# Kernel optimization log

Measured on AMD Instinct MI355X. Metric: run time of the kernel, lower is better.

The kernel has to match this reference:

```python
import jax, jax.numpy as jnp
import numpy as np

EMBED_DIM = 1024
N_HEADS = 16
HEAD_DIM = EMBED_DIM // N_HEADS

def setup_inputs() -> dict:
    key = jax.random.key(0)
    kx, kq, kk, kv, ko = jax.random.split(key, 5)
    s = 1.0 / np.sqrt(EMBED_DIM)
    return {
        "x": jax.random.normal(kx, (4, 2048, EMBED_DIM), dtype=jnp.float32),
        "Wq": jax.random.normal(kq, (EMBED_DIM, EMBED_DIM), dtype=jnp.float32) * s,
        "Wk": jax.random.normal(kk, (EMBED_DIM, EMBED_DIM), dtype=jnp.float32) * s,
        "Wv": jax.random.normal(kv, (EMBED_DIM, EMBED_DIM), dtype=jnp.float32) * s,
        "Wo": jax.random.normal(ko, (EMBED_DIM, EMBED_DIM), dtype=jnp.float32) * s,
    }

def reference(x, Wq, Wk, Wv, Wo):
    B, T, D = x.shape
    H, Dh = N_HEADS, HEAD_DIM
    # projections (nn.Linear: y = x @ W.T); split heads -> [B, H, T, Dh]
    Q = (x @ Wq.T).reshape(B, T, H, Dh).transpose(0, 2, 1, 3)
    K = (x @ Wk.T).reshape(B, T, H, Dh).transpose(0, 2, 1, 3)
    V = (x @ Wv.T).reshape(B, T, H, Dh).transpose(0, 2, 1, 3)
    scores = jnp.einsum("bhqd,bhkd->bhqk", Q, K) / jnp.sqrt(jnp.float32(Dh))
    attn = jax.nn.softmax(scores, axis=-1)
    out = jnp.einsum("bhqk,bhkd->bhqd", attn, V)  # [B,H,T,Dh]
    out = out.transpose(0, 2, 1, 3).reshape(B, T, D)
    return out @ Wo.T
```

## Files before the change

kernel.cpp:

```cpp
#include <hip/hip_runtime.h>

typedef _Float16 f16;
typedef _Float16 f16x8 __attribute__((ext_vector_type(8)));
typedef _Float16 f16x4 __attribute__((ext_vector_type(4)));
typedef float f32x4 __attribute__((ext_vector_type(4)));

#define MFMA16(a, b, c) __builtin_amdgcn_mfma_f32_16x16x32_f16((a), (b), (c), 0, 0, 0)
#define MEMBAR() __asm__ __volatile__("" ::: "memory")

__device__ __forceinline__ void cp16(const f16* g, f16* l) {
  __builtin_amdgcn_global_load_lds(
      (const __attribute__((address_space(1))) void*)g,
      (__attribute__((address_space(3))) void*)l, 16, 0, 0);
}

__global__ __launch_bounds__(256) void cvt_all(
    const float* __restrict__ x,  const float* __restrict__ Wq,
    const float* __restrict__ Wk, const float* __restrict__ Wv,
    const float* __restrict__ Wo,
    f16* __restrict__ X16, f16* __restrict__ Wq16, f16* __restrict__ Wk16,
    f16* __restrict__ Wv16, f16* __restrict__ Wo16) {
  int blk = blockIdx.x;
  const float* src; f16* dst; size_t off;
  if (blk < 4096) { src = x; dst = X16; off = (size_t)blk * 2048; }
  else {
    int t = blk - 4096, widx = t >> 9, loc = t & 511;
    src = (widx == 0) ? Wq : (widx == 1) ? Wk : (widx == 2) ? Wv : Wo;
    dst = (widx == 0) ? Wq16 : (widx == 1) ? Wk16 : (widx == 2) ? Wv16 : Wo16;
    off = (size_t)loc * 2048;
  }
  size_t e = off + (size_t)threadIdx.x * 8;
  const float4* s = (const float4*)(src + e);
  float4 a = s[0], b = s[1];
  f16x8 o;
  o[0] = (f16)a.x; o[1] = (f16)a.y; o[2] = (f16)a.z; o[3] = (f16)a.w;
  o[4] = (f16)b.x; o[5] = (f16)b.y; o[6] = (f16)b.z; o[7] = (f16)b.w;
  *(f16x8*)(dst + e) = o;
}

__device__ __forceinline__ void gemm_core(
    const f16* __restrict__ A, const f16* __restrict__ B, void* __restrict__ Cv,
    bool outF16, bool permT, int N, int K, int bm, int bn, float scale,
    f16* As, f16* Bs) {
  const int tid = threadIdx.x;
  const int lane = tid & 63, w = tid >> 6;
  const int wm = w >> 1, wn = w & 1;
  const int c = lane & 15, q = lane >> 4;
  const int key = (c >> 1) & 3;
  f32x4 acc[4][4] = {};

  const int Lrow = lane >> 2, Lp = (lane & 3) ^ ((lane >> 3) & 3);
  auto stage = [&](int k0, int bufi) {
#pragma unroll
    for (int j = 0; j < 2; ++j) {
      int r0 = (w * 2 + j) * 16;
      cp16(A + (size_t)(bm + r0 + Lrow) * K + k0 + Lp * 8,
           As + bufi * 4096 + r0 * 32 + lane * 8);
    }
#pragma unroll
    for (int j = 0; j < 2; ++j) {
      int r0 = (w * 2 + j) * 16;
      cp16(B + (size_t)(bn + r0 + Lrow) * K + k0 + Lp * 8,
           Bs + bufi * 4096 + r0 * 32 + lane * 8);
    }
  };

  stage(0, 0);
  const int NIT = K >> 5;
  for (int i = 0; i < NIT; ++i) {
    if (i + 1 < NIT) {
      stage((i + 1) << 5, (i + 1) & 1);
      __builtin_amdgcn_s_waitcnt(0x0F74);
    } else {
      __builtin_amdgcn_s_waitcnt(0x0F70);
    }
    __builtin_amdgcn_s_barrier();
    MEMBAR();
    const f16* Ab = As + (i & 1) * 4096;
    const f16* Bb = Bs + (i & 1) * 4096;
    f16x8 af[4], bf[4];
#pragma unroll
    for (int mt = 0; mt < 4; ++mt)
      af[mt] = *(const f16x8*)(Ab + (wm * 64 + mt * 16 + c) * 32 + (q ^ key) * 8);
#pragma unroll
    for (int nt = 0; nt < 4; ++nt)
      bf[nt] = *(const f16x8*)(Bb + (wn * 64 + nt * 16 + c) * 32 + (q ^ key) * 8);
#pragma unroll
    for (int mt = 0; mt < 4; ++mt)
#pragma unroll
      for (int nt = 0; nt < 4; ++nt)
        acc[mt][nt] = MFMA16(af[mt], bf[nt], acc[mt][nt]);
    MEMBAR();
    __builtin_amdgcn_s_barrier();
  }

#pragma unroll
  for (int mt = 0; mt < 4; ++mt)
#pragma unroll
    for (int nt = 0; nt < 4; ++nt)
#pragma unroll
      for (int r = 0; r < 4; ++r) {
        size_t row = bm + wm * 64 + mt * 16 + q * 4 + r;
        size_t col = bn + wn * 64 + nt * 16 + c;
        if (permT) {
          int t = (int)col & 63;
          col = (col & ~(size_t)63) |
                (size_t)((t & 0x23) | ((t & 0x0C) << 1) | ((t & 0x10) >> 2));
        }
        float v = acc[mt][nt][r] * scale;
        if (outF16) ((f16*)Cv)[row * N + col] = (f16)v;
        else ((float*)Cv)[row * N + col] = v;
      }
}

__global__ __launch_bounds__(256, 4) void gemm_qkvt(
    const f16* __restrict__ X, const f16* __restrict__ Wq,
    const f16* __restrict__ Wk, const f16* __restrict__ Wv,
    f16* __restrict__ Q, f16* __restrict__ Ko, f16* __restrict__ VT, float cs) {
  __shared__ __align__(16) f16 As[8192], Bs[8192];
  const int z = blockIdx.z, x = blockIdx.x;
  if (z < 2) {
    gemm_core(X, z ? Wk : Wq, z ? (void*)Ko : (void*)Q, true, false, 1024, 1024,
              (x >> 3) * 128, (x & 7) * 128, z ? 1.0f : cs, As, Bs);
  } else {
    gemm_core(Wv, X, (void*)VT, true, true, 8192, 1024,
              (x >> 6) * 128, (x & 63) * 128, 1.0f, As, Bs);
  }
}

__global__ __launch_bounds__(256, 4) void gemm_o(
    const f16* __restrict__ A, const f16* __restrict__ Wo, float* __restrict__ out) {
  __shared__ __align__(16) f16 As[8192], Bs[8192];
  const int x = blockIdx.x;
  gemm_core(A, Wo, (void*)out, false, false, 1024, 1024,
            (x >> 3) * 128, (x & 7) * 128, 1.0f, As, Bs);
}

__global__ __launch_bounds__(512, 4) void attn_kernel(
    const f16* __restrict__ Qg, const f16* __restrict__ Kg,
    const f16* __restrict__ VTg, f16* __restrict__ Og) {
  const int T = 2048, D = 1024;
  const int x = blockIdx.x;
  const int xcd = x & 7, rem = x >> 3;
  const int qt = rem & 7, grp = rem >> 3;
  const int bh = (grp << 3) | xcd;
  const int b = bh >> 4, h = bh & 15;
  const size_t base = ((size_t)b * T) * D + h * 64;
  const size_t baseV = (size_t)h * 64 * 8192 + (size_t)b * T;
  __shared__ __align__(16) f16 smem[16384];
  const int tid = threadIdx.x;
  const int lane = tid & 63, w = tid >> 6;
  const int c = lane & 15, q = lane >> 4;
  const int cx = c & 7;
  f16* Kb = smem;
  f16* Vb = smem + 8192;

#pragma unroll
  for (int j = 0; j < 4; ++j) {
    int cb = (w * 4 + j) * 64;
    int ch = cb + lane;
    int row = ch >> 3, p = (ch & 7) ^ (row & 7);
    cp16(Qg + base + (size_t)(qt * 256 + row) * D + p * 8, smem + cb * 8);
  }
  __syncthreads();
  f16x8 qf[2][2];
#pragma unroll
  for (int nt = 0; nt < 2; ++nt)
#pragma unroll
    for (int kh = 0; kh < 2; ++kh)
      qf[nt][kh] = *(const f16x8*)(smem + (w * 32 + nt * 16 + c) * 64 + ((kh * 4 + q) ^ cx) * 8);
  __syncthreads();

  float l_[2] = {0.f, 0.f};
  f32x4 o_[2][4] = {};

  auto stageKV = [&](int kv, int bufi) {
    f16* Ks = Kb + bufi * 4096;
    f16* Vt = Vb + bufi * 4096;
    int cb = w * 64;
    int ch = cb + lane;
    int row = ch >> 3, p = (ch & 7) ^ (row & 7);
    cp16(Kg + base + (size_t)(kv + row) * D + p * 8, Ks + cb * 8);
    cp16(VTg + baseV + (size_t)row * 8192 + kv + p * 8, Vt + cb * 8);
  };

  stageKV(0, 0);
  for (int i = 0; i < 32; ++i) {
    if (i < 31) {
      stageKV((i + 1) * 64, (i + 1) & 1);
      __builtin_amdgcn_s_waitcnt(0x0F72);
    } else {
      __builtin_amdgcn_s_waitcnt(0x0F70);
    }
    __builtin_amdgcn_s_barrier();

    f16* Ks = Kb + (i & 1) * 4096;
    f16* Vt = Vb + (i & 1) * 4096;

    f32x4 st[4][2] = {};
#pragma unroll
    for (int kh = 0; kh < 2; ++kh) {
      f16x8 kf[4];
#pragma unroll
      for (int mt = 0; mt < 4; ++mt)
        kf[mt] = *(const f16x8*)(Ks + (mt * 16 + c) * 64 + ((kh * 4 + q) ^ cx) * 8);
      __builtin_amdgcn_s_setprio(1);
#pragma unroll
      for (int mt = 0; mt < 4; ++mt)
#pragma unroll
        for (int g = 0; g < 2; ++g)
          st[mt][g] = MFMA16(kf[mt], qf[g][kh], st[mt][g]);
      __builtin_amdgcn_s_setprio(0);
    }

    f16x8 pf[2][2];
#pragma unroll
    for (int g = 0; g < 2; ++g) {
      float s = 0.f;
#pragma unroll
      for (int mt = 0; mt < 4; ++mt) {
        float p0 = __builtin_amdgcn_exp2f(st[mt][g][0]);
        float p1 = __builtin_amdgcn_exp2f(st[mt][g][1]);
        float p2 = __builtin_amdgcn_exp2f(st[mt][g][2]);
        float p3 = __builtin_amdgcn_exp2f(st[mt][g][3]);
        s += (p0 + p1) + (p2 + p3);
        int kc = mt >> 1, hh = (mt & 1) * 4;
        pf[g][kc][hh + 0] = (f16)p0; pf[g][kc][hh + 1] = (f16)p1;
        pf[g][kc][hh + 2] = (f16)p2; pf[g][kc][hh + 3] = (f16)p3;
      }
      l_[g] += s;
    }

    __builtin_amdgcn_s_setprio(1);
#pragma unroll
    for (int kc = 0; kc < 2; ++kc)
#pragma unroll
      for (int d = 0; d < 4; ++d) {
        f16x8 vf = *(const f16x8*)(Vt + (d * 16 + c) * 64 + ((kc * 4 + q) ^ cx) * 8);
        o_[0][d] = MFMA16(pf[0][kc], vf, o_[0][d]);
        o_[1][d] = MFMA16(pf[1][kc], vf, o_[1][d]);
      }
    __builtin_amdgcn_s_setprio(0);
    MEMBAR();
    __builtin_amdgcn_s_barrier();
  }

#pragma unroll
  for (int g = 0; g < 2; ++g) {
    l_[g] += __shfl_xor(l_[g], 16);
    l_[g] += __shfl_xor(l_[g], 32);
  }

#pragma unroll
  for (int g = 0; g < 2; ++g)
#pragma unroll
    for (int r = 0; r < 4; ++r) {
      float linv = 1.0f / __shfl(l_[g], q * 4 + r);
      size_t row = (size_t)qt * 256 + w * 32 + g * 16 + q * 4 + r;
#pragma unroll
      for (int d = 0; d < 4; ++d)
        Og[base + row * D + d * 16 + c] = (f16)(o_[g][d][r] * linv);
    }
}

extern "C" void kernel_launch(void* const* d_in, const int* in_sizes, int n_in,
                              void* d_out, int out_size, void* d_ws, size_t ws_size,
                              hipStream_t stream) {
  const float* x  = (const float*)d_in[0];
  const float* Wq = (const float*)d_in[1];
  const float* Wk = (const float*)d_in[2];
  const float* Wv = (const float*)d_in[3];
  const float* Wo = (const float*)d_in[4];
  char* ws = (char*)d_ws;
  const size_t MB = 1ull << 20;
  f16* X16  = (f16*)(ws + 0 * MB);
  f16* Wq16 = (f16*)(ws + 16 * MB);
  f16* Wk16 = (f16*)(ws + 18 * MB);
  f16* Wv16 = (f16*)(ws + 20 * MB);
  f16* Wo16 = (f16*)(ws + 22 * MB);
  f16* Q16  = (f16*)(ws + 24 * MB);
  f16* K16  = (f16*)(ws + 40 * MB);
  f16* VT16 = (f16*)(ws + 56 * MB);
  f16* A16  = (f16*)(ws + 72 * MB);

  const float cs = 0.18033688011112042f;

  cvt_all<<<6144, 256, 0, stream>>>(x, Wq, Wk, Wv, Wo,
                                    X16, Wq16, Wk16, Wv16, Wo16);

  gemm_qkvt<<<dim3(512, 1, 3), 256, 0, stream>>>(
      X16, Wq16, Wk16, Wv16, Q16, K16, VT16, cs);

  attn_kernel<<<dim3(512, 1, 1), 512, 0, stream>>>(Q16, K16, VT16, A16);

  gemm_o<<<512, 256, 0, stream>>>(A16, Wo16, (float*)d_out);
}
```

Baseline: 255.4 us.

## Use 4 waves with 64 query rows each in attention kernel

The attention kernel drops from 8 waves of 32 query rows to 4 waves of 64 query rows per block. Each loaded K/V fragment is then reused across four query sub-tiles instead of two. The 64-key step is split into two 32-key halves to keep register pressure bounded. The aim is fewer LDS reads per MFMA and less barrier overhead per key tile, at the cost of more registers per wave, fewer waves to hide latency, and each wave issuing twice the global-to-LDS copies.

```diff
diff --git a/kernel.cpp b/kernel.cpp
--- a/kernel.cpp
+++ b/kernel.cpp
@@ -136,7 +136,7 @@
             (x >> 3) * 128, (x & 7) * 128, 1.0f, As, Bs);
 }
 
-__global__ __launch_bounds__(512, 4) void attn_kernel(
+__global__ __launch_bounds__(256, 2) void attn_kernel(
     const f16* __restrict__ Qg, const f16* __restrict__ Kg,
     const f16* __restrict__ VTg, f16* __restrict__ Og) {
   const int T = 2048, D = 1024;
@@ -156,39 +156,48 @@
   f16* Vb = smem + 8192;
 
 #pragma unroll
-  for (int j = 0; j < 4; ++j) {
-    int cb = (w * 4 + j) * 64;
+  for (int j = 0; j < 8; ++j) {
+    int cb = (w * 8 + j) * 64;
     int ch = cb + lane;
     int row = ch >> 3, p = (ch & 7) ^ (row & 7);
     cp16(Qg + base + (size_t)(qt * 256 + row) * D + p * 8, smem + cb * 8);
   }
   __syncthreads();
-  f16x8 qf[2][2];
-#pragma unroll
-  for (int nt = 0; nt < 2; ++nt)
+  f16x8 qf[4][2];
+#pragma unroll
+  for (int g = 0; g < 4; ++g)
 #pragma unroll
     for (int kh = 0; kh < 2; ++kh)
-      qf[nt][kh] = *(const f16x8*)(smem + (w * 32 + nt * 16 + c) * 64 + ((kh * 4 + q) ^ cx) * 8);
+      qf[g][kh] = *(const f16x8*)(smem + (w * 64 + g * 16 + c) * 64 + ((kh * 4 + q) ^ cx) * 8);
   __syncthreads();
 
-  float l_[2] = {0.f, 0.f};
-  f32x4 o_[2][4] = {};
+  float l_[4] = {0.f, 0.f, 0.f, 0.f};
+  f32x4 o_[4][4] = {};
 
   auto stageKV = [&](int kv, int bufi) {
     f16* Ks = Kb + bufi * 4096;
     f16* Vt = Vb + bufi * 4096;
-    int cb = w * 64;
-    int ch = cb + lane;
-    int row = ch >> 3, p = (ch & 7) ^ (row & 7);
-    cp16(Kg + base + (size_t)(kv + row) * D + p * 8, Ks + cb * 8);
-    cp16(VTg + baseV + (size_t)row * 8192 + kv + p * 8, Vt + cb * 8);
+#pragma unroll
+    for (int j = 0; j < 2; ++j) {
+      int cb = (w * 2 + j) * 64;
+      int ch = cb + lane;
+      int row = ch >> 3, p = (ch & 7) ^ (row & 7);
+      cp16(Kg + base + (size_t)(kv + row) * D + p * 8, Ks + cb * 8);
+    }
+#pragma unroll
+    for (int j = 0; j < 2; ++j) {
+      int cb = (w * 2 + j) * 64;
+      int ch = cb + lane;
+      int row = ch >> 3, p = (ch & 7) ^ (row & 7);
+      cp16(VTg + baseV + (size_t)row * 8192 + kv + p * 8, Vt + cb * 8);
+    }
   };
 
   stageKV(0, 0);
   for (int i = 0; i < 32; ++i) {
     if (i < 31) {
       stageKV((i + 1) * 64, (i + 1) & 1);
-      __builtin_amdgcn_s_waitcnt(0x0F72);
+      __builtin_amdgcn_s_waitcnt(0x0F74);
     } else {
       __builtin_amdgcn_s_waitcnt(0x0F70);
     }
@@ -197,66 +206,69 @@
     f16* Ks = Kb + (i & 1) * 4096;
     f16* Vt = Vb + (i & 1) * 4096;
 
-    f32x4 st[4][2] = {};
-#pragma unroll
-    for (int kh = 0; kh < 2; ++kh) {
-      f16x8 kf[4];
-#pragma unroll
-      for (int mt = 0; mt < 4; ++mt)
-        kf[mt] = *(const f16x8*)(Ks + (mt * 16 + c) * 64 + ((kh * 4 + q) ^ cx) * 8);
+#pragma unroll
+    for (int hk = 0; hk < 2; ++hk) {
+      f32x4 st[2][4] = {};
+#pragma unroll
+      for (int kh = 0; kh < 2; ++kh) {
+        f16x8 kf[2];
+#pragma unroll
+        for (int mt = 0; mt < 2; ++mt)
+          kf[mt] = *(const f16x8*)(Ks + ((hk * 2 + mt) * 16 + c) * 64 + ((kh * 4 + q) ^ cx) * 8);
+        __builtin_amdgcn_s_setprio(1);
+#pragma unroll
+        for (int mt = 0; mt < 2; ++mt)
+#pragma unroll
+          for (int g = 0; g < 4; ++g)
+            st[mt][g] = MFMA16(kf[mt], qf[g][kh], st[mt][g]);
+        __builtin_amdgcn_s_setprio(0);
+      }
+
+      f16x8 pf[4];
+#pragma unroll
+      for (int g = 0; g < 4; ++g) {
+        float s = 0.f;
+#pragma unroll
+        for (int mt = 0; mt < 2; ++mt) {
+          float p0 = __builtin_amdgcn_exp2f(st[mt][g][0]);
+          float p1 = __builtin_amdgcn_exp2f(st[mt][g][1]);
+          float p2 = __builtin_amdgcn_exp2f(st[mt][g][2]);
+          float p3 = __builtin_amdgcn_exp2f(st[mt][g][3]);
+          s += (p0 + p1) + (p2 + p3);
+          int hh = mt * 4;
+          pf[g][hh + 0] = (f16)p0; pf[g][hh + 1] = (f16)p1;
+          pf[g][hh + 2] = (f16)p2; pf[g][hh + 3] = (f16)p3;
+        }
+        l_[g] += s;
+      }
+
       __builtin_amdgcn_s_setprio(1);
 #pragma unroll
-      for (int mt = 0; mt < 4; ++mt)
-#pragma unroll
-        for (int g = 0; g < 2; ++g)
-          st[mt][g] = MFMA16(kf[mt], qf[g][kh], st[mt][g]);
+      for (int d = 0; d < 4; ++d) {
+        f16x8 vf = *(const f16x8*)(Vt + (d * 16 + c) * 64 + ((hk * 4 + q) ^ cx) * 8);
+        o_[0][d] = MFMA16(pf[0], vf, o_[0][d]);
+        o_[1][d] = MFMA16(pf[1], vf, o_[1][d]);
+        o_[2][d] = MFMA16(pf[2], vf, o_[2][d]);
+        o_[3][d] = MFMA16(pf[3], vf, o_[3][d]);
+      }
       __builtin_amdgcn_s_setprio(0);
     }
-
-    f16x8 pf[2][2];
-#pragma unroll
-    for (int g = 0; g < 2; ++g) {
-      float s = 0.f;
-#pragma unroll
-      for (int mt = 0; mt < 4; ++mt) {
-        float p0 = __builtin_amdgcn_exp2f(st[mt][g][0]);
-        float p1 = __builtin_amdgcn_exp2f(st[mt][g][1]);
-        float p2 = __builtin_amdgcn_exp2f(st[mt][g][2]);
-        float p3 = __builtin_amdgcn_exp2f(st[mt][g][3]);
-        s += (p0 + p1) + (p2 + p3);
-        int kc = mt >> 1, hh = (mt & 1) * 4;
-        pf[g][kc][hh + 0] = (f16)p0; pf[g][kc][hh + 1] = (f16)p1;
-        pf[g][kc][hh + 2] = (f16)p2; pf[g][kc][hh + 3] = (f16)p3;
-      }
-      l_[g] += s;
-    }
-
-    __builtin_amdgcn_s_setprio(1);
-#pragma unroll
-    for (int kc = 0; kc < 2; ++kc)
-#pragma unroll
-      for (int d = 0; d < 4; ++d) {
-        f16x8 vf = *(const f16x8*)(Vt + (d * 16 + c) * 64 + ((kc * 4 + q) ^ cx) * 8);
-        o_[0][d] = MFMA16(pf[0][kc], vf, o_[0][d]);
-        o_[1][d] = MFMA16(pf[1][kc], vf, o_[1][d]);
-      }
-    __builtin_amdgcn_s_setprio(0);
     MEMBAR();
     __builtin_amdgcn_s_barrier();
   }
 
 #pragma unroll
-  for (int g = 0; g < 2; ++g) {
+  for (int g = 0; g < 4; ++g) {
     l_[g] += __shfl_xor(l_[g], 16);
     l_[g] += __shfl_xor(l_[g], 32);
   }
 
 #pragma unroll
-  for (int g = 0; g < 2; ++g)
+  for (int g = 0; g < 4; ++g)
 #pragma unroll
     for (int r = 0; r < 4; ++r) {
       float linv = 1.0f / __shfl(l_[g], q * 4 + r);
-      size_t row = (size_t)qt * 256 + w * 32 + g * 16 + q * 4 + r;
+      size_t row = (size_t)qt * 256 + w * 64 + g * 16 + q * 4 + r;
 #pragma unroll
       for (int d = 0; d < 4; ++d)
         Og[base + row * D + d * 16 + c] = (f16)(o_[g][d][r] * linv);
@@ -291,7 +303,7 @@
   gemm_qkvt<<<dim3(512, 1, 3), 256, 0, stream>>>(
       X16, Wq16, Wk16, Wv16, Q16, K16, VT16, cs);
 
-  attn_kernel<<<dim3(512, 1, 1), 512, 0, stream>>>(Q16, K16, VT16, A16);
+  attn_kernel<<<dim3(512, 1, 1), 256, 0, stream>>>(Q16, K16, VT16, A16);
 
   gemm_o<<<512, 256, 0, stream>>>(A16, Wo16, (float*)d_out);
 }
```

New measurement: 259.6 us. About the same (+1.6%).
